# Kernel optimization log

Hardware: AMD Instinct MI355X
Metric: run time of the kernel (lower is better)

Reference implementation:

```python
import jax, jax.numpy as jnp
import numpy as np
import math

B, T, N, IN_FEAT = 2, 64, 128, 2
H_LSTM = IN_FEAT * 2   # 4
D = IN_FEAT * 4        # 8
FH, FW = 16, 16
C_MAP = 2048
C_COMP = 32
TH = 0.5
IMG = 512.0


def setup_inputs() -> dict:
    key = jax.random.key(0)
    ks = jax.random.split(key, 20)
    s = 0.02
    inp = {
        "x": jax.random.uniform(ks[0], (B, 2, T, N), jnp.float32) * IMG,  # pixel coords in [0,512)
        "metadata": jax.random.normal(ks[1], (B, C_MAP, FH, FW), jnp.float32),
        # LSTM(in_feat, 2*in_feat): gates order i,f,g,o
        "w_ih": jax.random.normal(ks[2], (4 * H_LSTM, IN_FEAT), jnp.float32) * s,
        "w_hh": jax.random.normal(ks[3], (4 * H_LSTM, H_LSTM), jnp.float32) * s,
        "b_ih": jax.random.normal(ks[4], (4 * H_LSTM,), jnp.float32) * s,
        "b_hh": jax.random.normal(ks[5], (4 * H_LSTM,), jnp.float32) * s,
        "fc_w": jax.random.normal(ks[6], (D, H_LSTM), jnp.float32) * s,
        "fc_b": jax.random.normal(ks[7], (D,), jnp.float32) * s,
        "fc2_w": jax.random.normal(ks[8], (D, IN_FEAT), jnp.float32) * s,
        "fc2_b": jax.random.normal(ks[9], (D,), jnp.float32) * s,
        "fc3_w": jax.random.normal(ks[10], (D, IN_FEAT), jnp.float32) * s,
        "fc3_b": jax.random.normal(ks[11], (D,), jnp.float32) * s,
        "comp_w": jax.random.normal(ks[12], (C_COMP, C_MAP), jnp.float32) * s,
        "comp_b": jax.random.normal(ks[13], (C_COMP,), jnp.float32) * s,
        "vf_w": jax.random.normal(ks[14], (H_LSTM, H_LSTM + C_COMP), jnp.float32) * s,
        "vf_b": jax.random.normal(ks[15], (H_LSTM,), jnp.float32) * s,
        "fcout_w": jax.random.normal(ks[16], (IN_FEAT, D), jnp.float32) * s,
        "fcout_b": jax.random.normal(ks[17], (IN_FEAT,), jnp.float32) * s,
    }
    return inp


def _grid_sample_bilinear(fm, grid):
    # fm: [B,C,H,W]; grid: [B,P,1,2] normalized (x,y) in [-1,1]; bilinear, zeros padding, align_corners=False
    Bb, C, Hh, Ww = fm.shape
    gx, gy = grid[..., 0], grid[..., 1]              # [B,P,1]
    ix = ((gx + 1.0) * Ww - 1.0) * 0.5
    iy = ((gy + 1.0) * Hh - 1.0) * 0.5
    ix0 = jnp.floor(ix); iy0 = jnp.floor(iy)
    wx = ix - ix0; wy = iy - iy0

    def gather(f, yy, xx):
        valid = ((yy >= 0) & (yy < Hh) & (xx >= 0) & (xx < Ww)).astype(f.dtype)
        yc = jnp.clip(yy, 0, Hh - 1).astype(jnp.int32)
        xc = jnp.clip(xx, 0, Ww - 1).astype(jnp.int32)
        return f[:, yc, xc] * valid[None]            # [C,P,1]

    def per_batch(f, x0, y0, wx_, wy_):
        x1 = x0 + 1.0; y1 = y0 + 1.0
        return (gather(f, y0, x0) * ((1 - wy_) * (1 - wx_))[None]
                + gather(f, y0, x1) * ((1 - wy_) * wx_)[None]
                + gather(f, y1, x0) * (wy_ * (1 - wx_))[None]
                + gather(f, y1, x1) * (wy_ * wx_)[None])

    return jax.vmap(per_batch)(fm, ix0, iy0, wx, wy)  # [B,C,P,1]


def reference(x, metadata, w_ih, w_hh, b_ih, b_hh, fc_w, fc_b, fc2_w, fc2_b,
              fc3_w, fc3_b, comp_w, comp_b, vf_w, vf_b, fcout_w, fcout_b):
    coords = x                                        # [B,2,T,N] raw pixel coords
    xp = jnp.transpose(x, (0, 2, 3, 1))               # [B,T,N,2]
    b, t, n, c = xp.shape

    # sinusoidal positional encoding over time axis
    div = jnp.exp(jnp.arange(0, c, 2, dtype=jnp.float32) * (-math.log(10000.0) / c))
    pos = jnp.arange(t, dtype=jnp.float32)[:, None]
    pe = jnp.zeros((t, c), xp.dtype)
    pe = pe.at[:, 0::2].set(jnp.sin(pos * div))
    pe = pe.at[:, 1::2].set(jnp.cos(pos * div))
    xp = xp + pe[None, :, None, :]
    xr = xp.reshape(-1, c)                            # [M,2], M=b*t*n

    # single-step LSTM with zero init state (seq_len==1 in original)
    gates = xr @ w_ih.T + b_ih + b_hh                 # h0=0 => W_hh term vanishes
    i, f, g, o = jnp.split(gates, 4, axis=-1)
    cst = jax.nn.sigmoid(i) * jnp.tanh(g)
    X = jax.nn.sigmoid(o) * jnp.tanh(cst)             # [M,4]

    # visual fusion: 1x1 conv compressor + grid_sample local context
    comp = jnp.einsum('bchw,oc->bohw', metadata, comp_w) + comp_b[None, :, None, None]
    cgrid = jnp.transpose(coords, (0, 2, 3, 1)).reshape(b, -1, 1, 2)
    ngrid = 2.0 * (cgrid / IMG) - 1.0
    sampled = _grid_sample_bilinear(comp, ngrid)      # [B,32,TN,1]
    lc = jnp.transpose(sampled[..., 0], (0, 2, 1)).reshape(-1, C_COMP)  # [M,32]
    X = jnp.concatenate([X, lc], axis=-1) @ vf_w.T + vf_b               # [M,4]

    # sigmoid-gated full attention over all t*n tokens
    Q = (X @ fc_w.T + fc_b).reshape(b, t * n, -1)     # [B,TN,8]
    K = (xr @ fc2_w.T + fc2_b).reshape(b, t * n, -1)
    V = (xr @ fc3_w.T + fc3_b).reshape(b, t * n, -1)
    probs = jax.nn.sigmoid(jnp.einsum('bqd,bkd->bqk', Q, K))  # [B,TN,TN]
    out = jnp.einsum('bqk,bkd->bqd', probs, V).reshape(-1, Q.shape[-1])

    out = out * (out > TH).astype(out.dtype)          # threshold-ReLU
    out = out @ fcout_w.T + fcout_b                   # [M,2]
    out = out.reshape(b, t, n, -1)
    return jnp.transpose(out, (0, 3, 1, 2))           # [B,2,T,N]
```

## Files before the change

### kernel.cpp

```cpp
#include <hip/hip_runtime.h>
#include <math.h>

#define BB    2
#define TT    64
#define NN    128
#define TN    8192
#define MM    16384
#define CMAP  2048
#define CCOMP 32
#define FHW   256

#define CSPLIT 32
#define CRANGE 64
#define NCOMPB 64

#define DEG    17
#define NS     18
#define NODD   9
#define MDIM   19
#define NMOMF  (MDIM*MDIM)
#define MCH    64
#define MPTS   128
#define ZFIT   5.0
#define ZFITF  5.0f
#define UVBOUND 1.0045f

struct QCoef { float cb[NS][NODD]; };

#define OFF_CP    0
#define OFF_COMP  (OFF_CP + CSPLIT*BB*FHW*CCOMP)
#define OFF_X     (OFF_COMP + BB*FHW*CCOMP)
#define OFF_MP    (OFF_X + MM*2)

__device__ unsigned g_cdone;

__device__ __forceinline__ float fast_sigmoid(float v) {
    return __builtin_amdgcn_rcpf(1.0f + __expf(-v));
}
__device__ __forceinline__ float fast_tanh(float v) {
    return 1.0f - 2.0f * __builtin_amdgcn_rcpf(1.0f + __expf(2.0f * v));
}

__global__ void __launch_bounds__(256) k_pre(const float* __restrict__ x,
                                             const float* __restrict__ metadata,
                                             const float* __restrict__ comp_w,
                                             const float* __restrict__ comp_b,
                                             float* __restrict__ Cp,
                                             float* __restrict__ comp_ws,
                                             float2* __restrict__ Xr,
                                             float* __restrict__ Mp) {
    __shared__ float lds[2 * MPTS * MDIM];

    const int blk = blockIdx.x;
    const int tid = threadIdx.x;

    if (blk < NCOMPB) {
        const int b  = blk & 1;
        const int cs = blk >> 1;
        float (*wcs)[CCOMP] = (float(*)[CCOMP])lds;
        for (int i = tid; i < CRANGE * CCOMP; i += 256) {
            int c = i >> 5, o = i & 31;
            wcs[c][o] = comp_w[o * CMAP + cs * CRANGE + c];
        }
        __syncthreads();

        float acc[CCOMP];
#pragma unroll
        for (int o = 0; o < CCOMP; o++) acc[o] = 0.0f;

        const float* mb = metadata + ((size_t)b * CMAP + (size_t)cs * CRANGE) * FHW + tid;
#pragma unroll 4
        for (int c = 0; c < CRANGE; c++) {
            float mv = mb[c * FHW];
#pragma unroll
            for (int o = 0; o < CCOMP; o++) acc[o] += mv * wcs[c][o];
        }

        float* outp = Cp + (size_t)cs * (BB * FHW * CCOMP) + ((size_t)b * FHW + tid) * CCOMP;
#pragma unroll
        for (int o = 0; o < CCOMP; o += 4)
            *(float4*)&outp[o] = make_float4(acc[o], acc[o + 1], acc[o + 2], acc[o + 3]);

        __threadfence();
        __syncthreads();
        if (tid == 0) {
            unsigned my  = atomicAdd(&g_cdone, 1u);
            unsigned tgt = (my / NCOMPB + 1u) * NCOMPB;
            while (atomicAdd(&g_cdone, 0u) < tgt)
                __builtin_amdgcn_s_sleep(1);
        }
        __syncthreads();
        __threadfence();

        const int i = blk * 256 + tid;
        float s = 0.0f;
#pragma unroll 8
        for (int cs2 = 0; cs2 < CSPLIT; cs2++)
            s += Cp[(size_t)cs2 * (BB * FHW * CCOMP) + i];
        comp_ws[i] = s + comp_b[i & (CCOMP - 1)];
    } else {
        const int idx = blk - NCOMPB;
        const int b  = idx & 1;
        const int ch = idx >> 1;
        float (*spu)[MDIM] = (float(*)[MDIM])lds;
        float (*spv)[MDIM] = (float(*)[MDIM])(lds + MPTS * MDIM);

        if (tid < MPTS) {
            const int p = ch * MPTS + tid;
            const int t = p >> 7;
            const float px = x[(size_t)(b * 2 + 0) * TN + p];
            const float py = x[(size_t)(b * 2 + 1) * TN + p];
            const float xr0 = px + __sinf((float)t);
            const float xr1 = py + __cosf((float)t);
            Xr[b * TN + p] = make_float2(xr0, xr1);

            const float u = (xr0 - 256.0f) * (1.0f / 256.0f);
            const float v = (xr1 - 256.0f) * (1.0f / 256.0f);
            float a = 1.0f, c = 1.0f;
#pragma unroll
            for (int i = 0; i < MDIM; i++) {
                spu[tid][i] = a; spv[tid][i] = c;
                a *= u; c *= v;
            }
        }
        __syncthreads();

        float* outp = Mp + ((size_t)(b * MCH + ch)) * NMOMF;
        for (int i = tid; i < NMOMF; i += 256) {
            const int j = i / MDIM, l = i % MDIM;
            float s = 0.0f;
            if (j + l < MDIM) {
#pragma unroll 8
                for (int p = 0; p < MPTS; p++)
                    s += spu[p][j] * spv[p][l];
            }
            outp[i] = s;
        }
    }
}

__global__ void __launch_bounds__(256) k_main(
        const float* __restrict__ x,
        const float* __restrict__ w_ih,
        const float* __restrict__ b_ih,  const float* __restrict__ b_hh,
        const float* __restrict__ fc_w,  const float* __restrict__ fc_b,
        const float* __restrict__ fc2_w, const float* __restrict__ fc2_b,
        const float* __restrict__ fc3_w, const float* __restrict__ fc3_b,
        const float* __restrict__ vf_w,  const float* __restrict__ vf_b,
        const float* __restrict__ fcout_w, const float* __restrict__ fcout_b,
        const float* __restrict__ comp_ws,
        const float2* __restrict__ Xr,
        const float* __restrict__ Mp,
        float* __restrict__ y, QCoef qc) {
    __shared__ float sM[NMOMF];

    const int tid = threadIdx.x;
    const int m   = blockIdx.x * 256 + tid;
    const int b   = m >> 13;
    const int p   = m & (TN - 1);
    const int t   = p >> 7;

    for (int i = tid; i < NMOMF; i += 256) {
        float s = 0.0f;
#pragma unroll 16
        for (int ch = 0; ch < MCH; ch++)
            s += Mp[((size_t)(b * MCH + ch)) * NMOMF + i];
        sM[i] = s;
    }
    __syncthreads();

    const float px = x[(size_t)(b * 2 + 0) * TN + p];
    const float py = x[(size_t)(b * 2 + 1) * TN + p];
    const float xr0 = px + __sinf((float)t);
    const float xr1 = py + __cosf((float)t);

    float X[4];
#pragma unroll
    for (int j = 0; j < 4; j++) {
        float gi = xr0 * w_ih[(j)      * 2] + xr1 * w_ih[(j)      * 2 + 1] + b_ih[j]      + b_hh[j];
        float gg = xr0 * w_ih[(8 + j)  * 2] + xr1 * w_ih[(8 + j)  * 2 + 1] + b_ih[8 + j]  + b_hh[8 + j];
        float go = xr0 * w_ih[(12 + j) * 2] + xr1 * w_ih[(12 + j) * 2 + 1] + b_ih[12 + j] + b_hh[12 + j];
        float cst = fast_sigmoid(gi) * fast_tanh(gg);
        X[j] = fast_sigmoid(go) * fast_tanh(cst);
    }

    float lc[CCOMP];
#pragma unroll
    for (int c = 0; c < CCOMP; c++) lc[c] = 0.0f;

    const float ix = px * (1.0f / 32.0f) - 0.5f;
    const float iy = py * (1.0f / 32.0f) - 0.5f;
    const float fx0 = floorf(ix), fy0 = floorf(iy);
    const float wx = ix - fx0, wy = iy - fy0;
    const int x0 = (int)fx0, y0 = (int)fy0;
    const float* cb = comp_ws + (size_t)b * FHW * CCOMP;

#pragma unroll
    for (int dy = 0; dy < 2; dy++) {
#pragma unroll
        for (int dx = 0; dx < 2; dx++) {
            int xx = x0 + dx, yy = y0 + dy;
            if (xx < 0 || xx > 15 || yy < 0 || yy > 15) continue;
            float w = (dy ? wy : 1.0f - wy) * (dx ? wx : 1.0f - wx);
            const float4* cp4 = (const float4*)(cb + (yy * 16 + xx) * CCOMP);
#pragma unroll
            for (int c4 = 0; c4 < CCOMP / 4; c4++) {
                float4 v = cp4[c4];
                lc[c4 * 4 + 0] += w * v.x;
                lc[c4 * 4 + 1] += w * v.y;
                lc[c4 * 4 + 2] += w * v.z;
                lc[c4 * 4 + 3] += w * v.w;
            }
        }
    }

    float X2[4];
#pragma unroll
    for (int j = 0; j < 4; j++) {
        float a = vf_b[j];
#pragma unroll
        for (int k = 0; k < 4; k++) a += X[k] * vf_w[j * 36 + k];
#pragma unroll
        for (int c = 0; c < CCOMP; c++) a += lc[c] * vf_w[j * 36 + 4 + c];
        X2[j] = a;
    }

    float al = 0.0f, be = 0.0f, ga = 0.0f;
#pragma unroll
    for (int d = 0; d < 8; d++) {
        float q = fc_b[d];
#pragma unroll
        for (int k = 0; k < 4; k++) q += X2[k] * fc_w[d * 4 + k];
        al += q * fc2_b[d];
        be += q * fc2_w[d * 2];
        ga += q * fc2_w[d * 2 + 1];
    }

    const float b1 = 256.0f * be;
    const float c1 = 256.0f * ga;
    const float a0 = al + 256.0f * (be + ga);

    float S0, S1, S2;
    const float zb = fabsf(a0) + UVBOUND * (fabsf(b1) + fabsf(c1));
    if (zb >= ZFITF) {
        float s0 = 0.0f, s1 = 0.0f, s2 = 0.0f;
        const float2* xp = Xr + b * TN;
        for (int k = 0; k < TN; k++) {
            float2 kv = xp[k];
            float z = al + be * kv.x + ga * kv.y;
            float sg = fast_sigmoid(z);
            s0 += sg; s1 += sg * kv.x; s2 += sg * kv.y;
        }
        S0 = s0; S1 = s1; S2 = s2;
    } else {
        float pa[NS];
        pa[0] = 1.0f;
#pragma unroll
        for (int tt = 1; tt < NS; tt++) pa[tt] = pa[tt - 1] * a0;

        float A[NS];
#pragma unroll
        for (int s = 0; s < NS; s++) {
            float acc = 0.0f;
            const int t0 = (s & 1) ? 0 : 1;
#pragma unroll
            for (int q = 0; q < NODD; q++) {
                const int tt = t0 + 2 * q;
                if (s + tt <= DEG) acc = fmaf(qc.cb[s][q], pa[tt], acc);
            }
            A[s] = acc;
        }

        float R0 = A[0] * sM[0];
        float R1 = A[0] * sM[1 * MDIM + 0];
        float R2 = A[0] * sM[0 * MDIM + 1];

        float Ep[NS], Ec[NS];
        Ep[0] = 1.0f;
#pragma unroll
        for (int s = 1; s < NS; s++) {
            Ec[0] = c1 * Ep[0];
#pragma unroll
            for (int j = 1; j < NS; j++)
                if (j < s) Ec[j] = fmaf(b1, Ep[j - 1], c1 * Ep[j]);
            Ec[s] = b1 * Ep[s - 1];

            float W = 0.0f, W1 = 0.0f, W2 = 0.0f;
#pragma unroll
            for (int j = 0; j < NS; j++) {
                if (j <= s) {
                    const int l = s - j;
                    const float e = Ec[j];
                    W  = fmaf(e, sM[j * MDIM + l],       W);
                    W1 = fmaf(e, sM[(j + 1) * MDIM + l], W1);
                    W2 = fmaf(e, sM[j * MDIM + l + 1],   W2);
                }
            }
            R0 = fmaf(A[s], W,  R0);
            R1 = fmaf(A[s], W1, R1);
            R2 = fmaf(A[s], W2, R2);
#pragma unroll
            for (int j = 0; j < NS; j++)
                if (j <= s) Ep[j] = Ec[j];
        }

        S0 = 4096.0f + R0;
        const float su = 0.5f * sM[1 * MDIM + 0] + R1;
        const float sv = 0.5f * sM[0 * MDIM + 1] + R2;
        S1 = 256.0f * su + 256.0f * S0;
        S2 = 256.0f * sv + 256.0f * S0;
    }

    float f0 = fcout_b[0], f1 = fcout_b[1];
#pragma unroll
    for (int d = 0; d < 8; d++) {
        float vv = S0 * fc3_b[d] + S1 * fc3_w[d * 2] + S2 * fc3_w[d * 2 + 1];
        vv = (vv > 0.5f) ? vv : 0.0f;
        f0 += vv * fcout_w[d];
        f1 += vv * fcout_w[8 + d];
    }
    y[(size_t)(b * 2 + 0) * TN + p] = f0;
    y[(size_t)(b * 2 + 1) * TN + p] = f1;
}

static QCoef compute_qcoef() {
    const int NNODE = 64;
    const double PI = 3.14159265358979323846;
    double term[NODD];
    for (int i = 0; i < NODD; ++i) term[i] = 0.0;

    for (int jn = 0; jn < NNODE; ++jn) {
        double theta = (jn + 0.5) * (PI / NNODE);
        double ct = cos(theta);
        double zj = ZFIT * ct;
        double fj = 1.0 / (1.0 + exp(-zj)) - 0.5;
        double Ckm2 = 1.0, Ckm1 = ct;
        term[0] += fj * ct;
        int idx = 1;
        for (int k = 2; k <= DEG; ++k) {
            double Ck = 2.0 * ct * Ckm1 - Ckm2;
            Ckm2 = Ckm1; Ckm1 = Ck;
            if (k & 1) term[idx++] += fj * Ck;
        }
    }

    double c[DEG + 1];
    for (int i = 0; i <= DEG; ++i) c[i] = 0.0;
    for (int i = 0; i < NODD; ++i) c[2 * i + 1] = term[i] * (2.0 / NNODE);

    double Tm2[DEG + 1], Tm1[DEG + 1], a[DEG + 1];
    for (int i = 0; i <= DEG; ++i) { Tm2[i] = 0.0; Tm1[i] = 0.0; a[i] = 0.0; }
    Tm2[0] = 1.0; Tm1[1] = 1.0;
    a[1] = c[1];
    for (int k = 2; k <= DEG; ++k) {
        double Tc[DEG + 1];
        for (int mm = 0; mm <= DEG; ++mm) Tc[mm] = 0.0;
        for (int mm = 0; mm <= k; ++mm) {
            double vv = -Tm2[mm];
            if (mm > 0) vv += 2.0 * Tm1[mm - 1];
            Tc[mm] = vv;
        }
        if (k & 1)
            for (int mm = 1; mm <= k; mm += 2) a[mm] += c[k] * Tc[mm];
        for (int mm = 0; mm <= DEG; ++mm) { Tm2[mm] = Tm1[mm]; Tm1[mm] = Tc[mm]; }
    }

    double Cz[DEG + 1];
    double sc = 1.0;
    for (int mm = 0; mm <= DEG; ++mm) { Cz[mm] = a[mm] * sc; sc *= (1.0 / ZFIT); }

    double Bi[NS][NS];
    for (int n = 0; n < NS; ++n)
        for (int k = 0; k < NS; ++k) Bi[n][k] = 0.0;
    for (int n = 0; n < NS; ++n) {
        Bi[n][0] = 1.0;
        for (int k = 1; k <= n; ++k)
            Bi[n][k] = Bi[n - 1][k - 1] + ((k <= n - 1) ? Bi[n - 1][k] : 0.0);
    }

    QCoef qc;
    for (int s = 0; s < NS; ++s)
        for (int q = 0; q < NODD; ++q) qc.cb[s][q] = 0.0f;
    for (int s = 0; s < NS; ++s) {
        int q = 0;
        for (int t = (s & 1) ? 0 : 1; s + t <= DEG; t += 2)
            qc.cb[s][q++] = (float)(Cz[s + t] * Bi[s + t][s]);
    }
    return qc;
}

extern "C" void kernel_launch(void* const* d_in, const int* in_sizes, int n_in,
                              void* d_out, int out_size, void* d_ws, size_t ws_size,
                              hipStream_t stream) {
    const float* x        = (const float*)d_in[0];
    const float* metadata = (const float*)d_in[1];
    const float* w_ih     = (const float*)d_in[2];
    const float* b_ih     = (const float*)d_in[4];
    const float* b_hh     = (const float*)d_in[5];
    const float* fc_w     = (const float*)d_in[6];
    const float* fc_b     = (const float*)d_in[7];
    const float* fc2_w    = (const float*)d_in[8];
    const float* fc2_b    = (const float*)d_in[9];
    const float* fc3_w    = (const float*)d_in[10];
    const float* fc3_b    = (const float*)d_in[11];
    const float* comp_w   = (const float*)d_in[12];
    const float* comp_b   = (const float*)d_in[13];
    const float* vf_w     = (const float*)d_in[14];
    const float* vf_b     = (const float*)d_in[15];
    const float* fcout_w  = (const float*)d_in[16];
    const float* fcout_b  = (const float*)d_in[17];

    static const QCoef qc = compute_qcoef();

    float*  ws      = (float*)d_ws;
    float*  Cp      = ws + OFF_CP;
    float*  comp_ws = ws + OFF_COMP;
    float2* Xr      = (float2*)(ws + OFF_X);
    float*  Mp      = ws + OFF_MP;

    k_pre<<<192, 256, 0, stream>>>(x, metadata, comp_w, comp_b,
                                   Cp, comp_ws, Xr, Mp);

    k_main<<<64, 256, 0, stream>>>(x, w_ih, b_ih, b_hh,
                                   fc_w, fc_b, fc2_w, fc2_b,
                                   fc3_w, fc3_b, vf_w, vf_b,
                                   fcout_w, fcout_b,
                                   comp_ws, Xr, Mp, (float*)d_out, qc);
}
```

Baseline: 132.6 us.

## Replace split-K compressor with barrier and partial sums by per-output-channel blocks

The 1x1 compressor conv no longer splits channels across blocks with a workspace of partial sums and a spinning atomic grid barrier. Each block now computes one output channel for one batch across all 2048 input channels, writing the result directly. This removes the barrier, the partial-sum buffer and the reduction pass, but every block re-reads the whole metadata slab for its batch, multiplying memory traffic, and each thread runs a long serial dot product.

Result: slower. 159.3 us (+20.1%).

```diff
diff --git a/kernel.cpp b/kernel.cpp
--- a/kernel.cpp
+++ b/kernel.cpp
@@ -9,10 +9,6 @@
 #define CMAP  2048
 #define CCOMP 32
 #define FHW   256
-
-#define CSPLIT 32
-#define CRANGE 64
-#define NCOMPB 64
 
 #define DEG    17
 #define NS     18
@@ -27,12 +23,9 @@
 
 struct QCoef { float cb[NS][NODD]; };
 
-#define OFF_CP    0
-#define OFF_COMP  (OFF_CP + CSPLIT*BB*FHW*CCOMP)
+#define OFF_COMP  0
 #define OFF_X     (OFF_COMP + BB*FHW*CCOMP)
 #define OFF_MP    (OFF_X + MM*2)
-
-__device__ unsigned g_cdone;
 
 __device__ __forceinline__ float fast_sigmoid(float v) {
     return __builtin_amdgcn_rcpf(1.0f + __expf(-v));
@@ -45,7 +38,6 @@
                                              const float* __restrict__ metadata,
                                              const float* __restrict__ comp_w,
                                              const float* __restrict__ comp_b,
-                                             float* __restrict__ Cp,
                                              float* __restrict__ comp_ws,
                                              float2* __restrict__ Xr,
                                              float* __restrict__ Mp) {
@@ -54,52 +46,23 @@
     const int blk = blockIdx.x;
     const int tid = threadIdx.x;
 
-    if (blk < NCOMPB) {
-        const int b  = blk & 1;
-        const int cs = blk >> 1;
-        float (*wcs)[CCOMP] = (float(*)[CCOMP])lds;
-        for (int i = tid; i < CRANGE * CCOMP; i += 256) {
-            int c = i >> 5, o = i & 31;
-            wcs[c][o] = comp_w[o * CMAP + cs * CRANGE + c];
-        }
-        __syncthreads();
-
-        float acc[CCOMP];
-#pragma unroll
-        for (int o = 0; o < CCOMP; o++) acc[o] = 0.0f;
-
-        const float* mb = metadata + ((size_t)b * CMAP + (size_t)cs * CRANGE) * FHW + tid;
-#pragma unroll 4
-        for (int c = 0; c < CRANGE; c++) {
-            float mv = mb[c * FHW];
-#pragma unroll
-            for (int o = 0; o < CCOMP; o++) acc[o] += mv * wcs[c][o];
-        }
-
-        float* outp = Cp + (size_t)cs * (BB * FHW * CCOMP) + ((size_t)b * FHW + tid) * CCOMP;
-#pragma unroll
-        for (int o = 0; o < CCOMP; o += 4)
-            *(float4*)&outp[o] = make_float4(acc[o], acc[o + 1], acc[o + 2], acc[o + 3]);
-
-        __threadfence();
-        __syncthreads();
-        if (tid == 0) {
-            unsigned my  = atomicAdd(&g_cdone, 1u);
-            unsigned tgt = (my / NCOMPB + 1u) * NCOMPB;
-            while (atomicAdd(&g_cdone, 0u) < tgt)
-                __builtin_amdgcn_s_sleep(1);
-        }
-        __syncthreads();
-        __threadfence();
-
-        const int i = blk * 256 + tid;
-        float s = 0.0f;
+    if (blk < 64) {
+        const int b  = blk >> 5;
+        const int o  = blk & 31;
+        const int hw = tid;
+
+        const float* mb = metadata + (size_t)b * CMAP * FHW + hw;
+        const float* wr = comp_w + (size_t)o * CMAP;
+
+        float a0 = 0.0f, a1 = 0.0f;
 #pragma unroll 8
-        for (int cs2 = 0; cs2 < CSPLIT; cs2++)
-            s += Cp[(size_t)cs2 * (BB * FHW * CCOMP) + i];
-        comp_ws[i] = s + comp_b[i & (CCOMP - 1)];
+        for (int c = 0; c < CMAP; c += 2) {
+            a0 = fmaf(mb[(size_t)c * FHW],       wr[c],     a0);
+            a1 = fmaf(mb[(size_t)(c + 1) * FHW], wr[c + 1], a1);
+        }
+        comp_ws[((size_t)b * FHW + hw) * CCOMP + o] = a0 + a1 + comp_b[o];
     } else {
-        const int idx = blk - NCOMPB;
+        const int idx = blk - 64;
         const int b  = idx & 1;
         const int ch = idx >> 1;
         float (*spu)[MDIM] = (float(*)[MDIM])lds;
@@ -413,13 +376,12 @@
     static const QCoef qc = compute_qcoef();
 
     float*  ws      = (float*)d_ws;
-    float*  Cp      = ws + OFF_CP;
     float*  comp_ws = ws + OFF_COMP;
     float2* Xr      = (float2*)(ws + OFF_X);
     float*  Mp      = ws + OFF_MP;
 
     k_pre<<<192, 256, 0, stream>>>(x, metadata, comp_w, comp_b,
-                                   Cp, comp_ws, Xr, Mp);
+                                   comp_ws, Xr, Mp);
 
     k_main<<<64, 256, 0, stream>>>(x, w_ih, b_ih, b_hh,
                                    fc_w, fc_b, fc2_w, fc2_b,
```
